# Performance work log

Hardware: AMD Instinct MI355X
Metric: run time of the kernel (lower is better)

The kernel has to match this reference:

```python
import jax, jax.numpy as jnp
import numpy as np
import math

DIM = 384
NH = 6
DH = DIM // NH
B = 2
S = 2048
EPS = 1e-6
LN_EPS = 1e-5


def setup_inputs() -> dict:
    key = jax.random.key(0)
    ks = jax.random.split(key, 8)
    q = jax.random.normal(ks[0], (B, S, DIM), dtype=jnp.float32)
    k = jax.random.normal(ks[1], (B, S, DIM), dtype=jnp.float32)
    v = jax.random.normal(ks[2], (B, S, DIM), dtype=jnp.float32)
    # gate linear params (Linear(3*dim, num_heads)); small random weights to exercise the math
    igate_w = jax.random.normal(ks[3], (NH, 3 * DIM), dtype=jnp.float32) * 0.02
    igate_b = jax.random.normal(ks[4], (NH,), dtype=jnp.float32) * 0.1
    fgate_w = jax.random.normal(ks[5], (NH, 3 * DIM), dtype=jnp.float32) * 0.02
    fgate_b = jnp.linspace(3.0, 6.0, NH, dtype=jnp.float32)
    # MultiHeadLayerNorm residual weight (stored as delta, effective scale = 1 + w)
    outnorm_weight = jax.random.normal(ks[6], (DIM,), dtype=jnp.float32) * 0.02
    return {"q": q, "k": k, "v": v, "igate_w": igate_w, "igate_b": igate_b,
            "fgate_w": fgate_w, "fgate_b": fgate_b, "outnorm_weight": outnorm_weight}


def _mlstm_forward(q, k, v, igate_w, igate_b, fgate_w, fgate_b, outnorm_weight):
    Bq, Sq, _ = q.shape
    gate_in = jnp.concatenate([q, k, v], axis=-1)                       # (B,S,3D)
    ig = gate_in @ igate_w.T + igate_b                                   # (B,S,NH)
    fg = gate_in @ fgate_w.T + fgate_b                                   # (B,S,NH)
    # split heads: (B,NH,S,DH)
    qh = q.reshape(Bq, Sq, NH, DH).transpose(0, 2, 1, 3)
    kh = k.reshape(Bq, Sq, NH, DH).transpose(0, 2, 1, 3)
    vh = v.reshape(Bq, Sq, NH, DH).transpose(0, 2, 1, 3)
    ig = ig.transpose(0, 2, 1)                                           # (B,NH,S)
    fg = fg.transpose(0, 2, 1)                                           # (B,NH,S)

    log_fg = jax.nn.log_sigmoid(fg)                                      # (B,NH,S)
    lfc = jnp.concatenate([jnp.zeros((Bq, NH, 1), dtype=q.dtype),
                           jnp.cumsum(log_fg, axis=-1)], axis=-1)        # (B,NH,S+1)
    # log_fg_matrix[i,j] = cumsum[i] - cumsum[j] (sliced [1:,1:]), masked causal
    diff = lfc[:, :, 1:, None] - lfc[:, :, None, 1:]                     # (B,NH,S,S)
    ltr = jnp.tril(jnp.ones((Sq, Sq), dtype=bool))
    log_fg_mat = jnp.where(ltr, diff, -jnp.inf)
    log_D = log_fg_mat + ig[:, :, None, :]                               # + igate^T
    max_log_D = jnp.max(log_D, axis=-1, keepdims=True)                   # rowwise stabilize
    D = jnp.exp(log_D - max_log_D)
    qk = jnp.einsum('bhsd,bhtd->bhst', qh, kh) / math.sqrt(DH)
    C = qk * D
    normalizer = jnp.maximum(jnp.abs(jnp.sum(C, axis=-1, keepdims=True)),
                             jnp.exp(-max_log_D))
    h = jnp.einsum('bhst,bhtd->bhsd', C / (normalizer + EPS), vh)        # (B,NH,S,DH)

    # MultiHeadLayerNorm == group_norm over each head's DH channels, scale=(1+w)
    mean = jnp.mean(h, axis=-1, keepdims=True)
    var = jnp.var(h, axis=-1, keepdims=True)
    normed = (h - mean) / jnp.sqrt(var + LN_EPS)
    scale = (1.0 + outnorm_weight).reshape(NH, DH)[None, :, None, :]
    out = normed * scale
    return out.transpose(0, 2, 1, 3).reshape(Bq, Sq, DIM)


def reference(q, k, v, igate_w, igate_b, fgate_w, fgate_b, outnorm_weight):
    return _mlstm_forward(q, k, v, igate_w, igate_b, fgate_w, fgate_b, outnorm_weight)
```

## Files before the change

kernel.cpp:

```cpp
#include <hip/hip_runtime.h>
#include <math.h>

#define DIM 384
#define NH 6
#define DH 64
#define B_ 2
#define S_ 2048
#define EPS 1e-6f
#define LN_EPS 1e-5f
#define G3 (3*DIM)
#define LOG2E 1.44269504f
#define KSTR 72
#define NT (S_/64)
#define NSPLIT 4
#define NBH (B_*NH)
#define NGATE (B_*S_/4)

typedef __attribute__((ext_vector_type(8))) short bf16x8;
typedef __attribute__((ext_vector_type(4))) short bf16x4;
typedef __attribute__((ext_vector_type(4))) float f32x4;
typedef __attribute__((ext_vector_type(8))) unsigned short u16x8;

__device__ __forceinline__ unsigned short f2bf(float f){
    unsigned int u = __float_as_uint(f);
    u += 0x7fff + ((u >> 16) & 1);
    return (unsigned short)(u >> 16);
}
__device__ __forceinline__ float bf2f(unsigned short u){
    return __uint_as_float(((unsigned int)u) << 16);
}
__device__ __forceinline__ float logsig(float x){
    return fminf(x, 0.f) - log1pf(expf(-fabsf(x)));
}

__global__ __launch_bounds__(256) void gates_kernel(
    const float* __restrict__ q, const float* __restrict__ k, const float* __restrict__ v,
    const float* __restrict__ iw, const float* __restrict__ ib,
    const float* __restrict__ fw, const float* __restrict__ fb,
    float* __restrict__ ig_out, float* __restrict__ lf_out,
    unsigned short* __restrict__ Qb, unsigned short* __restrict__ Kb,
    unsigned short* __restrict__ Vt) {
    __shared__ unsigned short lt[64*KSTR];
    int tid = threadIdx.x;
    if (blockIdx.x >= NGATE){
        int lin = blockIdx.x - NGATE;
        int bh = lin / NT;
        int t0 = (lin % NT) * 64;
        int b = bh / NH, h = bh % NH;
        #pragma unroll
        for (int i = 0; i < 4; i++){
            int idx = tid + 256*i;
            int r = idx >> 4;
            int c4 = (idx & 15) * 4;
            float4 x = *(const float4*)(v + ((size_t)b*S_ + t0 + r)*DIM + h*DH + c4);
            lt[(c4+0)*KSTR + r] = f2bf(x.x);
            lt[(c4+1)*KSTR + r] = f2bf(x.y);
            lt[(c4+2)*KSTR + r] = f2bf(x.z);
            lt[(c4+3)*KSTR + r] = f2bf(x.w);
        }
        __syncthreads();
        #pragma unroll
        for (int i = 0; i < 2; i++){
            int idx = tid + 256*i;
            int d = idx >> 3;
            int t8 = (idx & 7) * 8;
            u16x8 o = *(const u16x8*)&lt[d*KSTR + t8];
            *(u16x8*)(Vt + (size_t)bh*DH*S_ + (size_t)d*S_ + t0 + t8) = o;
        }
        return;
    }
    int wave = (blockIdx.x * 256 + tid) >> 6;
    int lane = tid & 63;
    int b = wave / S_, s = wave % S_;
    size_t base = ((size_t)b * S_ + s) * DIM;
    float aI[NH], aF[NH];
    #pragma unroll
    for (int h = 0; h < NH; h++){ aI[h] = 0.f; aF[h] = 0.f; }
    for (int g = lane; g < G3/4; g += 64) {
        int e = g * 4;
        float4 x4;
        if (e < DIM){
            x4 = *(const float4*)(q + base + e);
            ushort4 t; t.x=f2bf(x4.x*0.125f); t.y=f2bf(x4.y*0.125f);
            t.z=f2bf(x4.z*0.125f); t.w=f2bf(x4.w*0.125f);
            *(ushort4*)(Qb + base + e) = t;
        } else if (e < 2*DIM){
            x4 = *(const float4*)(k + base + e - DIM);
            ushort4 t; t.x=f2bf(x4.x); t.y=f2bf(x4.y); t.z=f2bf(x4.z); t.w=f2bf(x4.w);
            *(ushort4*)(Kb + base + e - DIM) = t;
        } else {
            x4 = *(const float4*)(v + base + e - 2*DIM);
        }
        #pragma unroll
        for (int h = 0; h < NH; h++){
            float4 wi = *(const float4*)(iw + h*G3 + e);
            float4 wf = *(const float4*)(fw + h*G3 + e);
            aI[h] = fmaf(x4.x, wi.x, fmaf(x4.y, wi.y, fmaf(x4.z, wi.z, fmaf(x4.w, wi.w, aI[h]))));
            aF[h] = fmaf(x4.x, wf.x, fmaf(x4.y, wf.y, fmaf(x4.z, wf.z, fmaf(x4.w, wf.w, aF[h]))));
        }
    }
    #pragma unroll
    for (int h = 0; h < NH; h++){
        #pragma unroll
        for (int off = 32; off >= 1; off >>= 1){
            aI[h] += __shfl_xor(aI[h], off, 64);
            aF[h] += __shfl_xor(aF[h], off, 64);
        }
    }
    if (lane == 0) {
        #pragma unroll
        for (int h = 0; h < NH; h++){
            ig_out[((size_t)b*NH + h)*S_ + s] = aI[h] + ib[h];
            lf_out[((size_t)b*NH + h)*S_ + s] = logsig(aF[h] + fb[h]);
        }
    }
}

__global__ __launch_bounds__(256) void scan_kernel(
    const float* __restrict__ lf, const float* __restrict__ ig,
    float* __restrict__ cum, float* __restrict__ e2, float* __restrict__ pm,
    float* __restrict__ gA, float* __restrict__ baseA){
    int bh = blockIdx.x;
    const float* srcL = lf + (size_t)bh * S_;
    const float* srcI = ig + (size_t)bh * S_;
    float* dstC = cum + (size_t)bh * S_;
    float* dstE = e2 + (size_t)bh * S_;
    float* dstP = pm + (size_t)bh * S_;
    int tid = threadIdx.x;
    float loc[8];
    float run = 0.f;
    #pragma unroll
    for (int j = 0; j < 8; j++){ run += srcL[tid*8 + j]; loc[j] = run; }
    __shared__ float sm[256];
    sm[tid] = run;
    __syncthreads();
    float total = run;
    for (int off = 1; off < 256; off <<= 1){
        float vv = (tid >= off) ? sm[tid - off] : 0.f;
        __syncthreads();
        sm[tid] += vv;
        __syncthreads();
    }
    float excl = sm[tid] - total;
    float c[8];
    #pragma unroll
    for (int j = 0; j < 8; j++){ c[j] = excl + loc[j]; dstC[tid*8 + j] = c[j]; }
    __shared__ float sb[32];
    if ((tid & 7) == 0) sb[tid >> 3] = excl;
    __syncthreads();
    float base_t = sb[tid >> 3];
    float E[8], mloc = -INFINITY;
    #pragma unroll
    for (int j = 0; j < 8; j++){
        E[j] = srcI[tid*8 + j] - c[j] + base_t;
        dstE[tid*8 + j] = exp2f(E[j] * LOG2E);
        mloc = fmaxf(mloc, E[j]);
    }
    __shared__ float smax[256];
    smax[tid] = mloc;
    __syncthreads();
    float carry = -INFINITY;
    int g0 = tid & ~7;
    for (int u = g0; u < tid; u++) carry = fmaxf(carry, smax[u]);
    float runm = carry;
    #pragma unroll
    for (int j = 0; j < 8; j++){
        runm = fmaxf(runm, E[j]);
        dstP[tid*8 + j] = runm;
    }
    if ((tid & 7) == 7) gA[bh*NT + (tid >> 3)] = runm - base_t;
    if ((tid & 7) == 0) baseA[bh*NT + (tid >> 3)] = base_t;
}

__global__ __launch_bounds__(256) void mlstm_part(
    const unsigned short* __restrict__ Qb, const unsigned short* __restrict__ Kb,
    const unsigned short* __restrict__ Vt,
    const float* __restrict__ cum, const float* __restrict__ e2,
    const float* __restrict__ pm, const float* __restrict__ gA,
    const float* __restrict__ baseA,
    unsigned short* __restrict__ pOb, float* __restrict__ pM, float* __restrict__ pL) {
    int lin = blockIdx.x;
    int sp  = lin / NBH;
    int bh  = lin % NBH;
    int st  = (NT - 1) - (sp >> 2);
    int c   = sp & 3;
    int L   = (st + 4) >> 2;
    int tb0 = c * L;
    int tb1 = min((c + 1) * L, st + 1);
    int pblk = lin;
    int tid = threadIdx.x;

    if (tb0 >= tb1){
        if (tid < 64){ pM[pblk*64 + tid] = -INFINITY; pL[pblk*64 + tid] = 0.f; }
        return;
    }

    __shared__ unsigned short kt[2][64*KSTR];
    __shared__ unsigned short vt[2][64*KSTR];

    int b = bh / NH, h = bh % NH;
    int s0 = st * 64;
    int wv   = tid >> 6;
    int lane = tid & 63;
    int lq   = lane & 15;
    int quad = lane >> 4;

    const unsigned short* kbT = Kb + (size_t)b*S_*DIM + h*DH;
    const unsigned short* vtB = Vt + (size_t)bh*DH*S_;
    const float* cmb = cum + (size_t)bh*S_;
    const float* e2b = e2 + (size_t)bh*S_;
    const float* gB = gA + bh*NT;
    const float* baseB = baseA + bh*NT;

    int s_glob = s0 + 16*wv + lq;

    bf16x8 qf[2];
    {
        const unsigned short* qr = Qb + ((size_t)b*S_ + s_glob)*DIM + h*DH;
        qf[0] = *(const bf16x8*)(qr + 8*quad);
        qf[1] = *(const bf16x8*)(qr + 32 + 8*quad);
    }

    float cq   = cmb[s_glob];
    float pm_s = pm[(size_t)bh*S_ + s_glob];

    float m = -INFINITY;
    for (int tix = tb0; tix < tb1; tix++)
        if (tix != st) m = fmaxf(m, gB[tix]);
    if (tb1 == st + 1) m = fmaxf(m, pm_s - baseB[st]);
    float mn = cq + m;

    float b_loc = 0.f;
    f32x4 oacc[4];
    #pragma unroll
    for (int cg = 0; cg < 4; cg++) oacc[cg] = (f32x4){0.f,0.f,0.f,0.f};

    int sr[2], sc[2];
    #pragma unroll
    for (int i = 0; i < 2; i++){
        int idx = tid + 256*i;
        sr[i] = idx >> 3;
        sc[i] = (idx & 7) * 8;
    }

    u16x8 kreg[2], vreg[2];
    {
        const unsigned short* kb = kbT + (size_t)(tb0*64)*DIM;
        const unsigned short* vb = vtB + tb0*64;
        #pragma unroll
        for (int i = 0; i < 2; i++){
            kreg[i] = *(const u16x8*)(kb + (size_t)sr[i]*DIM + sc[i]);
            vreg[i] = *(const u16x8*)(vb + (size_t)sr[i]*S_ + sc[i]);
        }
        #pragma unroll
        for (int i = 0; i < 2; i++){
            *(u16x8*)&kt[0][sr[i]*KSTR + sc[i]] = kreg[i];
            *(u16x8*)&vt[0][sr[i]*KSTR + sc[i]] = vreg[i];
        }
    }
    __syncthreads();

    int bufi = 0;
    for (int t0 = tb0*64; t0 < tb1*64; t0 += 64){
        bool more = (t0 + 64 < tb1*64);
        if (more){
            const unsigned short* kb = kbT + (size_t)(t0 + 64)*DIM;
            const unsigned short* vb = vtB + (t0 + 64);
            #pragma unroll
            for (int i = 0; i < 2; i++){
                kreg[i] = *(const u16x8*)(kb + (size_t)sr[i]*DIM + sc[i]);
                vreg[i] = *(const u16x8*)(vb + (size_t)sr[i]*S_ + sc[i]);
            }
        }

        int tix = t0 >> 6;
        float base_t = baseB[tix];
        float ws = exp2f(-(m + base_t) * LOG2E);
        float4 e2v[4];
        #pragma unroll
        for (int tb = 0; tb < 4; tb++)
            e2v[tb] = *(const float4*)(e2b + t0 + 16*tb + 4*quad);

        const unsigned short* ktc = kt[bufi];
        const unsigned short* vtc = vt[bufi];
        f32x4 st4[4];
        #pragma unroll
        for (int tb = 0; tb < 4; tb++) st4[tb] = (f32x4){0.f,0.f,0.f,0.f};
        #pragma unroll
        for (int ks = 0; ks < 2; ks++){
            #pragma unroll
            for (int tb = 0; tb < 4; tb++){
                bf16x8 af = *(const bf16x8*)&ktc[(16*tb + lq)*KSTR + 32*ks + 8*quad];
                st4[tb] = __builtin_amdgcn_mfma_f32_16x16x32_bf16(af, qf[ks], st4[tb], 0, 0, 0);
            }
        }

        bool diag = (t0 == s0);
        float pv[4][4];
        #pragma unroll
        for (int tb = 0; tb < 4; tb++)
            #pragma unroll
            for (int r = 0; r < 4; r++)
                pv[tb][r] = st4[tb][r] * (ws * e2v[tb][r]);
        if (diag){
            #pragma unroll
            for (int tb = 0; tb < 4; tb++)
                #pragma unroll
                for (int r = 0; r < 4; r++)
                    if (t0 + 16*tb + 4*quad + r > s_glob) pv[tb][r] = 0.f;
        }
        bf16x4 pf[4];
        #pragma unroll
        for (int tb = 0; tb < 4; tb++){
            #pragma unroll
            for (int r = 0; r < 4; r++){
                b_loc += pv[tb][r];
                pf[tb][r] = (short)f2bf(pv[tb][r]);
            }
        }

        #pragma unroll
        for (int tb = 0; tb < 4; tb++){
            #pragma unroll
            for (int cg = 0; cg < 4; cg++){
                bf16x4 vf = *(const bf16x4*)&vtc[(16*cg + lq)*KSTR + 16*tb + 4*quad];
                oacc[cg] = __builtin_amdgcn_mfma_f32_16x16x16bf16_1k(pf[tb], vf, oacc[cg], 0, 0, 0);
            }
        }

        if (more){
            #pragma unroll
            for (int i = 0; i < 2; i++){
                *(u16x8*)&kt[bufi^1][sr[i]*KSTR + sc[i]] = kreg[i];
                *(u16x8*)&vt[bufi^1][sr[i]*KSTR + sc[i]] = vreg[i];
            }
            __syncthreads();
            bufi ^= 1;
        }
    }

    b_loc += __shfl_xor(b_loc, 16, 64);
    b_loc += __shfl_xor(b_loc, 32, 64);
    unsigned short* po = pOb + (size_t)pblk * 4096;
    #pragma unroll
    for (int r = 0; r < 4; r++){
        int row = 16*wv + 4*quad + r;
        #pragma unroll
        for (int cg = 0; cg < 4; cg++)
            po[row*64 + 16*cg + lq] = f2bf(oacc[cg][r]);
    }
    if (quad == 0){
        pM[pblk*64 + 16*wv + lq] = mn;
        pL[pblk*64 + 16*wv + lq] = b_loc;
    }
}

__global__ __launch_bounds__(256) void mlstm_combine(
    const unsigned short* __restrict__ pOb, const float* __restrict__ pM,
    const float* __restrict__ pL, const float* __restrict__ w,
    float* __restrict__ out) {
    int st = blockIdx.x;
    int bh = blockIdx.y;
    int b = bh / NH, h = bh % NH;
    int tid = threadIdx.x;
    int cl = (tid & 15) * 4;
    int rb = tid >> 4;

    int pblk[NSPLIT];
    #pragma unroll
    for (int p = 0; p < NSPLIT; p++)
        pblk[p] = (((NT - 1 - st) << 2) + p) * NBH + bh;

    float4 wv4 = *(const float4*)(w + h*DH + cl);

    #pragma unroll
    for (int pass = 0; pass < 4; pass++){
        int row = pass*16 + rb;
        float mp[NSPLIT], lp[NSPLIT];
        float mmax = -INFINITY;
        #pragma unroll
        for (int p = 0; p < NSPLIT; p++){
            mp[p] = pM[pblk[p]*64 + row];
            lp[p] = pL[pblk[p]*64 + row];
            mmax = fmaxf(mmax, mp[p]);
        }
        float l = 0.f;
        float ox = 0.f, oy = 0.f, oz = 0.f, ow = 0.f;
        #pragma unroll
        for (int p = 0; p < NSPLIT; p++){
            if (mp[p] != -INFINITY){
                float wp = exp2f((mp[p] - mmax) * LOG2E);
                l += wp * lp[p];
                ushort4 t4 = *(const ushort4*)(pOb + (size_t)pblk[p]*4096 + row*64 + cl);
                ox += wp*bf2f(t4.x); oy += wp*bf2f(t4.y);
                oz += wp*bf2f(t4.z); ow += wp*bf2f(t4.w);
            }
        }
        float nrm = fmaxf(fabsf(l), exp2f(-mmax * LOG2E));
        float inv = 1.f / (nrm + EPS);
        float x[4] = {ox*inv, oy*inv, oz*inv, ow*inv};
        float s1 = x[0]+x[1]+x[2]+x[3];
        float s2 = x[0]*x[0]+x[1]*x[1]+x[2]*x[2]+x[3]*x[3];
        #pragma unroll
        for (int off = 8; off >= 1; off >>= 1){
            s1 += __shfl_xor(s1, off, 64);
            s2 += __shfl_xor(s2, off, 64);
        }
        float mean = s1 * (1.f/64.f);
        float var  = s2 * (1.f/64.f) - mean*mean;
        float rstd = rsqrtf(var + LN_EPS);
        float4 oo;
        oo.x = (x[0]-mean)*rstd*(1.f + wv4.x);
        oo.y = (x[1]-mean)*rstd*(1.f + wv4.y);
        oo.z = (x[2]-mean)*rstd*(1.f + wv4.z);
        oo.w = (x[3]-mean)*rstd*(1.f + wv4.w);
        *(float4*)(out + ((size_t)b*S_ + st*64 + row)*DIM + h*DH + cl) = oo;
    }
}

extern "C" void kernel_launch(void* const* d_in, const int* in_sizes, int n_in,
                              void* d_out, int out_size, void* d_ws, size_t ws_size,
                              hipStream_t stream) {
    const float* q  = (const float*)d_in[0];
    const float* k  = (const float*)d_in[1];
    const float* v  = (const float*)d_in[2];
    const float* iw = (const float*)d_in[3];
    const float* ib = (const float*)d_in[4];
    const float* fw = (const float*)d_in[5];
    const float* fb = (const float*)d_in[6];
    const float* w  = (const float*)d_in[7];
    float* out = (float*)d_out;

    const int nPart = NBH * NT * NSPLIT;
    const size_t NE = (size_t)B_ * S_ * DIM;
    float* ig   = (float*)d_ws;
    float* lf   = ig   + (size_t)NBH*S_;
    float* cum  = lf   + (size_t)NBH*S_;
    float* e2   = cum  + (size_t)NBH*S_;
    float* pm   = e2   + (size_t)NBH*S_;
    float* gA   = pm   + (size_t)NBH*S_;
    float* base = gA   + (size_t)NBH*NT;
    float* pM   = base + (size_t)NBH*NT;
    float* pL   = pM   + (size_t)nPart*64;
    unsigned short* pOb = (unsigned short*)(pL + (size_t)nPart*64);
    unsigned short* Qb  = pOb + (size_t)nPart*4096;
    unsigned short* Kb  = Qb + NE;
    unsigned short* Vt  = Kb + NE;

    gates_kernel<<<NGATE + NBH*NT, 256, 0, stream>>>(q, k, v, iw, ib, fw, fb,
                                                     ig, lf, Qb, Kb, Vt);
    scan_kernel<<<NBH, 256, 0, stream>>>(lf, ig, cum, e2, pm, gA, base);
    mlstm_part<<<nPart, 256, 0, stream>>>(Qb, Kb, Vt, cum, e2, pm, gA, base, pOb, pM, pL);
    mlstm_combine<<<dim3(NT, NBH), 256, 0, stream>>>(pOb, pM, pL, w, out);
}
```

Before: 128.2 us.

## Process 128-row query tiles per block to reuse K/V tiles across two sub-tiles

Each mlstm_part block now handles two 64-row query sub-tiles (128 rows) against each staged K/V tile, halving the number of K/V loads into shared memory per query row and halving the partial-block count. The partial output buffers and the combine kernel are resized to 128 rows per block. It also packs probabilities to bf16 with the hip_bfloat162 intrinsic. The cost is more registers per thread (two accumulator sets), which may lower occupancy, and fewer blocks in the grid.

```diff
diff --git a/kernel.cpp b/kernel.cpp
--- a/kernel.cpp
+++ b/kernel.cpp
@@ -1,4 +1,5 @@
 #include <hip/hip_runtime.h>
+#include <hip/hip_bf16.h>
 #include <math.h>
 
 #define DIM 384
@@ -12,6 +13,7 @@
 #define LOG2E 1.44269504f
 #define KSTR 72
 #define NT (S_/64)
+#define NT2 (S_/128)
 #define NSPLIT 4
 #define NBH (B_*NH)
 #define NGATE (B_*S_/4)
@@ -31,6 +33,12 @@
 }
 __device__ __forceinline__ float logsig(float x){
     return fminf(x, 0.f) - log1pf(expf(-fabsf(x)));
+}
+__device__ __forceinline__ bf16x4 pack4(float a, float b, float c, float d){
+    union { __hip_bfloat162 h2[2]; bf16x4 v; } u;
+    u.h2[0] = __float22bfloat162_rn(make_float2(a, b));
+    u.h2[1] = __float22bfloat162_rn(make_float2(c, d));
+    return u.v;
 }
 
 __global__ __launch_bounds__(256) void gates_kernel(
@@ -182,16 +190,17 @@
     int lin = blockIdx.x;
     int sp  = lin / NBH;
     int bh  = lin % NBH;
-    int st  = (NT - 1) - (sp >> 2);
+    int qt  = (NT2 - 1) - (sp >> 2);
     int c   = sp & 3;
-    int L   = (st + 4) >> 2;
+    int ntile = 2*qt + 2;
+    int L   = (ntile + 3) >> 2;
     int tb0 = c * L;
-    int tb1 = min((c + 1) * L, st + 1);
+    int tb1 = min((c + 1) * L, ntile);
     int pblk = lin;
     int tid = threadIdx.x;
 
     if (tb0 >= tb1){
-        if (tid < 64){ pM[pblk*64 + tid] = -INFINITY; pL[pblk*64 + tid] = 0.f; }
+        if (tid < 128){ pM[pblk*128 + tid] = -INFINITY; pL[pblk*128 + tid] = 0.f; }
         return;
     }
 
@@ -199,7 +208,7 @@
     __shared__ unsigned short vt[2][64*KSTR];
 
     int b = bh / NH, h = bh % NH;
-    int s0 = st * 64;
+    int s0 = qt * 128;
     int wv   = tid >> 6;
     int lane = tid & 63;
     int lq   = lane & 15;
@@ -212,28 +221,29 @@
     const float* gB = gA + bh*NT;
     const float* baseB = baseA + bh*NT;
 
-    int s_glob = s0 + 16*wv + lq;
-
-    bf16x8 qf[2];
-    {
-        const unsigned short* qr = Qb + ((size_t)b*S_ + s_glob)*DIM + h*DH;
-        qf[0] = *(const bf16x8*)(qr + 8*quad);
-        qf[1] = *(const bf16x8*)(qr + 32 + 8*quad);
-    }
-
-    float cq   = cmb[s_glob];
-    float pm_s = pm[(size_t)bh*S_ + s_glob];
-
-    float m = -INFINITY;
-    for (int tix = tb0; tix < tb1; tix++)
-        if (tix != st) m = fmaxf(m, gB[tix]);
-    if (tb1 == st + 1) m = fmaxf(m, pm_s - baseB[st]);
-    float mn = cq + m;
-
-    float b_loc = 0.f;
-    f32x4 oacc[4];
-    #pragma unroll
-    for (int cg = 0; cg < 4; cg++) oacc[cg] = (f32x4){0.f,0.f,0.f,0.f};
+    int s_glob[2];
+    bf16x8 qf[2][2];
+    float cq[2], m[2], mn[2], b_loc[2];
+    f32x4 oacc[2][4];
+    #pragma unroll
+    for (int ss = 0; ss < 2; ss++){
+        s_glob[ss] = s0 + 64*ss + 16*wv + lq;
+        const unsigned short* qr = Qb + ((size_t)b*S_ + s_glob[ss])*DIM + h*DH;
+        qf[ss][0] = *(const bf16x8*)(qr + 8*quad);
+        qf[ss][1] = *(const bf16x8*)(qr + 32 + 8*quad);
+        cq[ss] = cmb[s_glob[ss]];
+        float pm_s = pm[(size_t)bh*S_ + s_glob[ss]];
+        int dg = 2*qt + ss;
+        float mm = -INFINITY;
+        int hi = min(tb1, dg + 1);
+        for (int tix = tb0; tix < hi; tix++)
+            mm = fmaxf(mm, (tix == dg) ? (pm_s - baseB[tix]) : gB[tix]);
+        m[ss] = mm;
+        mn[ss] = cq[ss] + mm;
+        b_loc[ss] = 0.f;
+        #pragma unroll
+        for (int cg = 0; cg < 4; cg++) oacc[ss][cg] = (f32x4){0.f,0.f,0.f,0.f};
+    }
 
     int sr[2], sc[2];
     #pragma unroll
@@ -275,7 +285,6 @@
 
         int tix = t0 >> 6;
         float base_t = baseB[tix];
-        float ws = exp2f(-(m + base_t) * LOG2E);
         float4 e2v[4];
         #pragma unroll
         for (int tb = 0; tb < 4; tb++)
@@ -283,48 +292,53 @@
 
         const unsigned short* ktc = kt[bufi];
         const unsigned short* vtc = vt[bufi];
-        f32x4 st4[4];
-        #pragma unroll
-        for (int tb = 0; tb < 4; tb++) st4[tb] = (f32x4){0.f,0.f,0.f,0.f};
-        #pragma unroll
-        for (int ks = 0; ks < 2; ks++){
-            #pragma unroll
-            for (int tb = 0; tb < 4; tb++){
-                bf16x8 af = *(const bf16x8*)&ktc[(16*tb + lq)*KSTR + 32*ks + 8*quad];
-                st4[tb] = __builtin_amdgcn_mfma_f32_16x16x32_bf16(af, qf[ks], st4[tb], 0, 0, 0);
-            }
-        }
-
-        bool diag = (t0 == s0);
-        float pv[4][4];
-        #pragma unroll
-        for (int tb = 0; tb < 4; tb++)
-            #pragma unroll
-            for (int r = 0; r < 4; r++)
-                pv[tb][r] = st4[tb][r] * (ws * e2v[tb][r]);
-        if (diag){
+
+        #pragma unroll
+        for (int ss = 0; ss < 2; ss++){
+            int dg = 2*qt + ss;
+            if (tix > dg) continue;
+            float ws = exp2f(-(m[ss] + base_t) * LOG2E);
+
+            f32x4 st4[4];
+            #pragma unroll
+            for (int tb = 0; tb < 4; tb++) st4[tb] = (f32x4){0.f,0.f,0.f,0.f};
+            #pragma unroll
+            for (int ks = 0; ks < 2; ks++){
+                #pragma unroll
+                for (int tb = 0; tb < 4; tb++){
+                    bf16x8 af = *(const bf16x8*)&ktc[(16*tb + lq)*KSTR + 32*ks + 8*quad];
+                    st4[tb] = __builtin_amdgcn_mfma_f32_16x16x32_bf16(af, qf[ss][ks], st4[tb], 0, 0, 0);
+                }
+            }
+
+            bool diag = (tix == dg);
+            float pv[4][4];
             #pragma unroll
             for (int tb = 0; tb < 4; tb++)
                 #pragma unroll
                 for (int r = 0; r < 4; r++)
-                    if (t0 + 16*tb + 4*quad + r > s_glob) pv[tb][r] = 0.f;
-        }
-        bf16x4 pf[4];
-        #pragma unroll
-        for (int tb = 0; tb < 4; tb++){
-            #pragma unroll
-            for (int r = 0; r < 4; r++){
-                b_loc += pv[tb][r];
-                pf[tb][r] = (short)f2bf(pv[tb][r]);
-            }
-        }
-
-        #pragma unroll
-        for (int tb = 0; tb < 4; tb++){
-            #pragma unroll
-            for (int cg = 0; cg < 4; cg++){
-                bf16x4 vf = *(const bf16x4*)&vtc[(16*cg + lq)*KSTR + 16*tb + 4*quad];
-                oacc[cg] = __builtin_amdgcn_mfma_f32_16x16x16bf16_1k(pf[tb], vf, oacc[cg], 0, 0, 0);
+                    pv[tb][r] = st4[tb][r] * (ws * e2v[tb][r]);
+            if (diag){
+                #pragma unroll
+                for (int tb = 0; tb < 4; tb++)
+                    #pragma unroll
+                    for (int r = 0; r < 4; r++)
+                        if (t0 + 16*tb + 4*quad + r > s_glob[ss]) pv[tb][r] = 0.f;
+            }
+            bf16x4 pf[4];
+            #pragma unroll
+            for (int tb = 0; tb < 4; tb++){
+                b_loc[ss] += (pv[tb][0] + pv[tb][1]) + (pv[tb][2] + pv[tb][3]);
+                pf[tb] = pack4(pv[tb][0], pv[tb][1], pv[tb][2], pv[tb][3]);
+            }
+
+            #pragma unroll
+            for (int tb = 0; tb < 4; tb++){
+                #pragma unroll
+                for (int cg = 0; cg < 4; cg++){
+                    bf16x4 vf = *(const bf16x4*)&vtc[(16*cg + lq)*KSTR + 16*tb + 4*quad];
+                    oacc[ss][cg] = __builtin_amdgcn_mfma_f32_16x16x16bf16_1k(pf[tb], vf, oacc[ss][cg], 0, 0, 0);
+                }
             }
         }
 
@@ -339,19 +353,22 @@
         }
     }
 
-    b_loc += __shfl_xor(b_loc, 16, 64);
-    b_loc += __shfl_xor(b_loc, 32, 64);
-    unsigned short* po = pOb + (size_t)pblk * 4096;
-    #pragma unroll
-    for (int r = 0; r < 4; r++){
-        int row = 16*wv + 4*quad + r;
-        #pragma unroll
-        for (int cg = 0; cg < 4; cg++)
-            po[row*64 + 16*cg + lq] = f2bf(oacc[cg][r]);
-    }
-    if (quad == 0){
-        pM[pblk*64 + 16*wv + lq] = mn;
-        pL[pblk*64 + 16*wv + lq] = b_loc;
+    unsigned short* po = pOb + (size_t)pblk * 8192;
+    #pragma unroll
+    for (int ss = 0; ss < 2; ss++){
+        b_loc[ss] += __shfl_xor(b_loc[ss], 16, 64);
+        b_loc[ss] += __shfl_xor(b_loc[ss], 32, 64);
+        #pragma unroll
+        for (int r = 0; r < 4; r++){
+            int row = 64*ss + 16*wv + 4*quad + r;
+            #pragma unroll
+            for (int cg = 0; cg < 4; cg++)
+                po[row*64 + 16*cg + lq] = f2bf(oacc[ss][cg][r]);
+        }
+        if (quad == 0){
+            pM[pblk*128 + 64*ss + 16*wv + lq] = mn[ss];
+            pL[pblk*128 + 64*ss + 16*wv + lq] = b_loc[ss];
+        }
     }
 }
 
@@ -359,7 +376,7 @@
     const unsigned short* __restrict__ pOb, const float* __restrict__ pM,
     const float* __restrict__ pL, const float* __restrict__ w,
     float* __restrict__ out) {
-    int st = blockIdx.x;
+    int qt = blockIdx.x;
     int bh = blockIdx.y;
     int b = bh / NH, h = bh % NH;
     int tid = threadIdx.x;
@@ -369,19 +386,19 @@
     int pblk[NSPLIT];
     #pragma unroll
     for (int p = 0; p < NSPLIT; p++)
-        pblk[p] = (((NT - 1 - st) << 2) + p) * NBH + bh;
+        pblk[p] = (((NT2 - 1 - qt) << 2) + p) * NBH + bh;
 
     float4 wv4 = *(const float4*)(w + h*DH + cl);
 
     #pragma unroll
-    for (int pass = 0; pass < 4; pass++){
+    for (int pass = 0; pass < 8; pass++){
         int row = pass*16 + rb;
         float mp[NSPLIT], lp[NSPLIT];
         float mmax = -INFINITY;
         #pragma unroll
         for (int p = 0; p < NSPLIT; p++){
-            mp[p] = pM[pblk[p]*64 + row];
-            lp[p] = pL[pblk[p]*64 + row];
+            mp[p] = pM[pblk[p]*128 + row];
+            lp[p] = pL[pblk[p]*128 + row];
             mmax = fmaxf(mmax, mp[p]);
         }
         float l = 0.f;
@@ -391,7 +408,7 @@
             if (mp[p] != -INFINITY){
                 float wp = exp2f((mp[p] - mmax) * LOG2E);
                 l += wp * lp[p];
-                ushort4 t4 = *(const ushort4*)(pOb + (size_t)pblk[p]*4096 + row*64 + cl);
+                ushort4 t4 = *(const ushort4*)(pOb + (size_t)pblk[p]*8192 + row*64 + cl);
                 ox += wp*bf2f(t4.x); oy += wp*bf2f(t4.y);
                 oz += wp*bf2f(t4.z); ow += wp*bf2f(t4.w);
             }
@@ -414,7 +431,7 @@
         oo.y = (x[1]-mean)*rstd*(1.f + wv4.y);
         oo.z = (x[2]-mean)*rstd*(1.f + wv4.z);
         oo.w = (x[3]-mean)*rstd*(1.f + wv4.w);
-        *(float4*)(out + ((size_t)b*S_ + st*64 + row)*DIM + h*DH + cl) = oo;
+        *(float4*)(out + ((size_t)b*S_ + qt*128 + row)*DIM + h*DH + cl) = oo;
     }
 }
 
@@ -431,7 +448,7 @@
     const float* w  = (const float*)d_in[7];
     float* out = (float*)d_out;
 
-    const int nPart = NBH * NT * NSPLIT;
+    const int nPart = NBH * NT2 * NSPLIT;
     const size_t NE = (size_t)B_ * S_ * DIM;
     float* ig   = (float*)d_ws;
     float* lf   = ig   + (size_t)NBH*S_;
@@ -441,9 +458,9 @@
     float* gA   = pm   + (size_t)NBH*S_;
     float* base = gA   + (size_t)NBH*NT;
     float* pM   = base + (size_t)NBH*NT;
-    float* pL   = pM   + (size_t)nPart*64;
-    unsigned short* pOb = (unsigned short*)(pL + (size_t)nPart*64);
-    unsigned short* Qb  = pOb + (size_t)nPart*4096;
+    float* pL   = pM   + (size_t)nPart*128;
+    unsigned short* pOb = (unsigned short*)(pL + (size_t)nPart*128);
+    unsigned short* Qb  = pOb + (size_t)nPart*8192;
     unsigned short* Kb  = Qb + NE;
     unsigned short* Vt  = Kb + NE;
 
@@ -451,5 +468,5 @@
                                                      ig, lf, Qb, Kb, Vt);
     scan_kernel<<<NBH, 256, 0, stream>>>(lf, ig, cum, e2, pm, gA, base);
     mlstm_part<<<nPart, 256, 0, stream>>>(Qb, Kb, Vt, cum, e2, pm, gA, base, pOb, pM, pL);
-    mlstm_combine<<<dim3(NT, NBH), 256, 0, stream>>>(pOb, pM, pL, w, out);
-}
+    mlstm_combine<<<dim3(NT2, NBH), 256, 0, stream>>>(pOb, pM, pL, w, out);
+}
```

New measurement: 138.5 us. +8.1%, slower.
